# Kernel optimization log

Hardware: AMD Instinct MI355X
Metric: run time of the kernel (lower is better)

The kernel has to match this reference:

```python
import jax, jax.numpy as jnp
import numpy as np

V, N = 3, 32768
C2, C3 = 256, 32          # feat_ch_2D, feat_ch_3D
H = W = 128               # 2D feature map size
D = 32                    # 3D volume feature size
CIN = C2 + C3             # 288, MLP in_channels


def setup_inputs() -> dict:
    key = jax.random.key(0)
    ks = jax.random.split(key, 16)
    sc = 0.02
    inp = {
        'pts': jax.random.uniform(ks[0], (1, N, 3), minval=-0.5, maxval=0.5),
        'pts_proj': jax.random.uniform(ks[1], (1, N, 2), minval=-1.0, maxval=1.0),
        'img_feat0': jax.random.normal(ks[2], (V, C2, H, W)),
        'img_feat1': jax.random.normal(ks[3], (V, C2, H, W)),
        'vol_feat0': jax.random.normal(ks[4], (V, C3, D, D, D)),
        'vol_feat1': jax.random.normal(ks[5], (V, C3, D, D, D)),
        'W0': jax.random.normal(ks[6], (1024, CIN)) * sc,  'b0': jnp.zeros((1024,)),
        'W1': jax.random.normal(ks[7], (512, CIN + 1024)) * sc, 'b1': jnp.zeros((512,)),
        'W2': jax.random.normal(ks[8], (256, CIN + 512)) * sc,  'b2': jnp.zeros((256,)),
        'W3': jax.random.normal(ks[9], (128, CIN + 256)) * sc,  'b3': jnp.zeros((128,)),
        'W4': jax.random.normal(ks[10], (1, 128)) * sc,         'b4': jnp.zeros((1,)),
        'mean_num': 3,
    }
    return inp


def _gs2d(feat, gx, gy):
    # feat: [C,H,W]; gx,gy: [N] normalized coords in [-1,1]
    C, Hh, Ww = feat.shape
    ix = jnp.clip(((gx + 1.0) * Ww - 1.0) * 0.5, 0.0, Ww - 1.0)  # align_corners=False, border pad
    iy = jnp.clip(((gy + 1.0) * Hh - 1.0) * 0.5, 0.0, Hh - 1.0)
    x0f, y0f = jnp.floor(ix), jnp.floor(iy)
    wx, wy = ix - x0f, iy - y0f
    x0 = x0f.astype(jnp.int32); x1 = jnp.minimum(x0 + 1, Ww - 1)
    y0 = y0f.astype(jnp.int32); y1 = jnp.minimum(y0 + 1, Hh - 1)
    v00 = feat[:, y0, x0]; v01 = feat[:, y0, x1]
    v10 = feat[:, y1, x0]; v11 = feat[:, y1, x1]
    return (v00 * (1 - wy) * (1 - wx) + v01 * (1 - wy) * wx
            + v10 * wy * (1 - wx) + v11 * wy * wx)  # [C,N]


def _gs3d(feat, gx, gy, gz):
    # feat: [C,D,H,W]; grid x->W, y->H, z->D (torch grid_sample convention)
    C, Dd, Hh, Ww = feat.shape
    ix = jnp.clip(((gx + 1.0) * Ww - 1.0) * 0.5, 0.0, Ww - 1.0)
    iy = jnp.clip(((gy + 1.0) * Hh - 1.0) * 0.5, 0.0, Hh - 1.0)
    iz = jnp.clip(((gz + 1.0) * Dd - 1.0) * 0.5, 0.0, Dd - 1.0)
    x0f, y0f, z0f = jnp.floor(ix), jnp.floor(iy), jnp.floor(iz)
    wx, wy, wz = ix - x0f, iy - y0f, iz - z0f
    x0 = x0f.astype(jnp.int32); x1 = jnp.minimum(x0 + 1, Ww - 1)
    y0 = y0f.astype(jnp.int32); y1 = jnp.minimum(y0 + 1, Hh - 1)
    z0 = z0f.astype(jnp.int32); z1 = jnp.minimum(z0 + 1, Dd - 1)
    def g(zi, yi, xi):
        return feat[:, zi, yi, xi]  # [C,N]
    out = (g(z0, y0, x0) * (1 - wz) * (1 - wy) * (1 - wx)
           + g(z0, y0, x1) * (1 - wz) * (1 - wy) * wx
           + g(z0, y1, x0) * (1 - wz) * wy * (1 - wx)
           + g(z0, y1, x1) * (1 - wz) * wy * wx
           + g(z1, y0, x0) * wz * (1 - wy) * (1 - wx)
           + g(z1, y0, x1) * wz * (1 - wy) * wx
           + g(z1, y1, x0) * wz * wy * (1 - wx)
           + g(z1, y1, x1) * wz * wy * wx)
    return out  # [C,N]


def _lrelu(x):
    return jnp.where(x >= 0, x, 0.2 * x)


def _conv1x1(Wm, bm, x):
    # x: [V,C,N] -> [V,O,N]
    return jnp.einsum('oc,vcn->von', Wm, x) + bm[None, :, None]


def _mlp0(x, W0, b0, W1, b1, W2, b2, W3, b3):
    out = _lrelu(_conv1x1(W0, b0, x))
    out = _lrelu(_conv1x1(W1, b1, jnp.concatenate([x, out], axis=1)))
    out = _lrelu(_conv1x1(W2, b2, jnp.concatenate([x, out], axis=1)))
    out = _lrelu(_conv1x1(W3, b3, jnp.concatenate([x, out], axis=1)))
    return out  # [V,128,N]


def _forward(pts, pts_proj, img_feats, vol_feats,
             W0, b0, W1, b1, W2, b2, W3, b3, W4, b4, mean_num):
    v = img_feats[0].shape[0]
    gx2 = jnp.broadcast_to(pts_proj[:, :, 0], (v, pts_proj.shape[1]))
    gy2 = jnp.broadcast_to(pts_proj[:, :, 1], (v, pts_proj.shape[1]))
    p = pts * 2.0  # pts *= 2.0 before 3D sampling
    gx3 = jnp.broadcast_to(p[:, :, 0], (v, p.shape[1]))
    gy3 = jnp.broadcast_to(p[:, :, 1], (v, p.shape[1]))
    gz3 = jnp.broadcast_to(p[:, :, 2], (v, p.shape[1]))
    outs = []
    for img_feat, vol_feat in zip(img_feats, vol_feats):
        f2 = jax.vmap(_gs2d)(img_feat, gx2, gy2)            # [V,C2,N]
        f3 = jax.vmap(_gs3d)(vol_feat, gx3, gy3, gz3)       # [V,C3,N]
        pt_feat = jnp.concatenate([f2, f3], axis=1)         # [V,288,N]
        pt_out0 = _mlp0(pt_feat, W0, b0, W1, b1, W2, b2, W3, b3)
        pt_out0_mean = jnp.mean(pt_out0[:mean_num], axis=0, keepdims=True)  # [1,128,N]
        sdf = jax.nn.sigmoid(_conv1x1(W4, b4, pt_out0_mean))                # [1,1,N]
        outs.append(jnp.transpose(sdf, (0, 2, 1)))                          # [1,N,1]
    return tuple(outs)


def reference(pts, pts_proj, img_feat0, img_feat1, vol_feat0, vol_feat1,
              W0, b0, W1, b1, W2, b2, W3, b3, W4, b4, mean_num):
    return _forward(pts, pts_proj, [img_feat0, img_feat1], [vol_feat0, vol_feat1],
                    W0, b0, W1, b1, W2, b2, W3, b3, W4, b4, mean_num)
```

## Files before the change

### kernel.cpp

```cpp
#include <hip/hip_runtime.h>
#include <hip/hip_bf16.h>

#define NV 3
#define NPTS 32768
#define C2C 256
#define C3C 32
#define CINC 288
#define CINP 320
#define HH 128
#define WWW 128
#define DDD 32

typedef short bh8 __attribute__((ext_vector_type(8)));
typedef float fx4 __attribute__((ext_vector_type(4)));
typedef unsigned short us4 __attribute__((ext_vector_type(4)));

__device__ __forceinline__ float b2f(unsigned short u) {
    unsigned int x = ((unsigned int)u) << 16;
    return __uint_as_float(x);
}
__device__ __forceinline__ unsigned short f2b(float f) {
    unsigned int x = __float_as_uint(f);
    unsigned int r = (x + 0x7FFFu + ((x >> 16) & 1u)) >> 16;
    return (unsigned short)r;
}

__device__ __forceinline__ void gl2lds16(const unsigned short* g, unsigned short* l) {
    __builtin_amdgcn_global_load_lds(
        (const __attribute__((address_space(1))) unsigned int*)g,
        (__attribute__((address_space(3))) unsigned int*)l, 16, 0, 0);
}

__device__ __forceinline__ int xcd_swz(int orig, int nwg) {
    int xcd = orig & 7;
    int q = nwg >> 3, r = nwg & 7;
    int base = (xcd < r) ? xcd * (q + 1) : r * (q + 1) + (xcd - r) * q;
    return base + (orig >> 3);
}

__global__ void k_wpad(const float* __restrict__ src, unsigned short* __restrict__ dst, int M, int Kp) {
    int idx = blockIdx.x * 256 + threadIdx.x;
    if (idx >= M * Kp) return;
    int m = idx / Kp, k = idx - m * Kp;
    int Ksrc = Kp - 32;
    float v;
    if (k < CINC) v = src[(size_t)m * Ksrc + k];
    else if (k < CINP) v = 0.0f;
    else v = src[(size_t)m * Ksrc + (k - 32)];
    dst[idx] = f2b(v);
}

__global__ void k_timg(const float* __restrict__ in, unsigned short* __restrict__ out) {
    int v = blockIdx.x >> 7, y = blockIdx.x & 127;
    int x0 = blockIdx.y << 6, c0 = blockIdx.z << 6;
    __shared__ float t[64][65];
    int tx = threadIdx.x & 63, tg = threadIdx.x >> 6;
    const float* src = in + (((size_t)(v * C2C + c0) * HH + y) * WWW + x0);
#pragma unroll
    for (int i = 0; i < 16; i++) {
        int cl = tg * 16 + i;
        t[cl][tx] = src[(size_t)cl * (HH * WWW) + tx];
    }
    __syncthreads();
    unsigned short* dst = out + ((size_t)(v * HH + y) * WWW + x0) * C2C + c0;
#pragma unroll
    for (int i = 0; i < 16; i++) {
        int xl = tg * 16 + i;
        dst[(size_t)xl * C2C + tx] = f2b(t[tx][xl]);
    }
}

__global__ void k_tvol(const float* __restrict__ in, unsigned short* __restrict__ out) {
    int v = blockIdx.x;
    int s0 = blockIdx.y << 8;
    __shared__ float t[32][257];
    int tid = threadIdx.x;
    const float* src = in + (size_t)v * C3C * 32768 + s0;
#pragma unroll
    for (int c = 0; c < 32; c++) t[c][tid] = src[(size_t)c * 32768 + tid];
    __syncthreads();
    unsigned short* dst = out + ((size_t)v * 32768 + s0) * C3C;
    int c = tid & 31, sb = tid >> 5;
#pragma unroll
    for (int j = 0; j < 32; j++) {
        int sl = j * 8 + sb;
        dst[(size_t)sl * C3C + c] = f2b(t[c][sl]);
    }
}

__global__ __launch_bounds__(256) void k_sample(const float* __restrict__ pts, const float* __restrict__ proj,
                         const unsigned short* __restrict__ imgT, const unsigned short* __restrict__ volT,
                         unsigned short* __restrict__ ptT, int n0, int Nk) {
    int w = threadIdx.x >> 6, l = threadIdx.x & 63;
    int i = blockIdx.x * 4 + w;
    int v = blockIdx.y;
    int n = n0 + i;
    unsigned short* dstRow = ptT + (size_t)(v * Nk + i) * CINP;

    {
        float gx = proj[n * 2 + 0], gy = proj[n * 2 + 1];
        float ix = fminf(fmaxf(((gx + 1.0f) * (float)WWW - 1.0f) * 0.5f, 0.0f), (float)(WWW - 1));
        float iy = fminf(fmaxf(((gy + 1.0f) * (float)HH - 1.0f) * 0.5f, 0.0f), (float)(HH - 1));
        float x0f = floorf(ix), y0f = floorf(iy);
        float wx = ix - x0f, wy = iy - y0f;
        int x0 = (int)x0f, y0 = (int)y0f;
        int x1 = min(x0 + 1, WWW - 1), y1 = min(y0 + 1, HH - 1);
        const unsigned short* base = imgT + (size_t)v * HH * WWW * C2C;
        us4 a = *((const us4*)(base + ((size_t)(y0 * WWW + x0)) * C2C) + l);
        us4 b = *((const us4*)(base + ((size_t)(y0 * WWW + x1)) * C2C) + l);
        us4 c = *((const us4*)(base + ((size_t)(y1 * WWW + x0)) * C2C) + l);
        us4 d = *((const us4*)(base + ((size_t)(y1 * WWW + x1)) * C2C) + l);
        float w00 = (1.0f - wy) * (1.0f - wx), w01 = (1.0f - wy) * wx;
        float w10 = wy * (1.0f - wx), w11 = wy * wx;
        us4 rv;
#pragma unroll
        for (int r = 0; r < 4; r++) {
            float f = b2f(a[r]) * w00 + b2f(b[r]) * w01 + b2f(c[r]) * w10 + b2f(d[r]) * w11;
            rv[r] = f2b(f);
        }
        *(us4*)(dstRow + l * 4) = rv;
    }
    {
        float gx = pts[n * 3 + 0] * 2.0f, gy = pts[n * 3 + 1] * 2.0f, gz = pts[n * 3 + 2] * 2.0f;
        float ix = fminf(fmaxf(((gx + 1.0f) * (float)DDD - 1.0f) * 0.5f, 0.0f), (float)(DDD - 1));
        float iy = fminf(fmaxf(((gy + 1.0f) * (float)DDD - 1.0f) * 0.5f, 0.0f), (float)(DDD - 1));
        float iz = fminf(fmaxf(((gz + 1.0f) * (float)DDD - 1.0f) * 0.5f, 0.0f), (float)(DDD - 1));
        float x0f = floorf(ix), y0f = floorf(iy), z0f = floorf(iz);
        float wx = ix - x0f, wy = iy - y0f, wz = iz - z0f;
        int x0 = (int)x0f, y0 = (int)y0f, z0 = (int)z0f;
        int x1 = min(x0 + 1, DDD - 1), y1 = min(y0 + 1, DDD - 1), z1 = min(z0 + 1, DDD - 1);
        int c = l & 31, zs = l >> 5;
        int zi = zs ? z1 : z0;
        float wzs = zs ? wz : (1.0f - wz);
        const unsigned short* base = volT + (size_t)v * 32768 * C3C;
        float f00 = b2f(base[((size_t)((zi * 32 + y0) * 32 + x0)) * C3C + c]);
        float f01 = b2f(base[((size_t)((zi * 32 + y0) * 32 + x1)) * C3C + c]);
        float f10 = b2f(base[((size_t)((zi * 32 + y1) * 32 + x0)) * C3C + c]);
        float f11 = b2f(base[((size_t)((zi * 32 + y1) * 32 + x1)) * C3C + c]);
        float r = (f00 * (1.0f - wy) * (1.0f - wx) + f01 * (1.0f - wy) * wx +
                   f10 * wy * (1.0f - wx) + f11 * wy * wx) * wzs;
        float other = __shfl_xor(r, 32);
        r += other;
        if (zs == 0) dstRow[C2C + c] = f2b(r);
    }
    if (l < 8) *(us4*)(dstRow + CINC + l * 4) = (us4){0, 0, 0, 0};
}

template <int K1, int K2, int M>
__device__ __forceinline__ void gemm128_body(const unsigned short* __restrict__ A,
                                             const unsigned short* __restrict__ B1,
                                             const unsigned short* __restrict__ B2,
                                             const float* __restrict__ bias,
                                             unsigned short* __restrict__ C) {
    constexpr int K = K1 + K2;
    __shared__ unsigned short Ash[128 * 32];
    __shared__ unsigned short Bsh[128 * 32];
    int tid = threadIdx.x;
    int w = tid >> 6, l = tid & 63;
    int la = l & 15, lg = l >> 4;
    int wm = w & 1, wn = w >> 1;
    int gx = gridDim.x;
    int nwg = gx * gridDim.y;
    int bid = xcd_swz(blockIdx.y * gx + blockIdx.x, nwg);
    int mBlk = (bid % gx) * 128;
    int nBlk = (bid / gx) * 128;

    int sRow = l >> 2;
    int sCol = (l & 3) * 8;

    fx4 acc[4][4];
#pragma unroll
    for (int mi = 0; mi < 4; mi++)
#pragma unroll
        for (int ni = 0; ni < 4; ni++) acc[mi][ni] = (fx4){0.f, 0.f, 0.f, 0.f};

    const unsigned short* Ag = A + (size_t)mBlk * K;
    {
        const unsigned short* Bg = B1 + (size_t)nBlk * K1;
        for (int k0 = 0; k0 < K1; k0 += 32) {
#pragma unroll
            for (int j = 0; j < 2; j++) {
                int r = w * 32 + j * 16 + sRow;
                gl2lds16(Ag + (size_t)r * K + k0 + sCol, &Ash[r * 32 + sCol]);
                gl2lds16(Bg + (size_t)r * K1 + k0 + sCol, &Bsh[r * 32 + sCol]);
            }
            __syncthreads();
            bh8 af[4], bfv[4];
#pragma unroll
            for (int mi = 0; mi < 4; mi++) af[mi] = *(const bh8*)&Ash[(wm * 64 + mi * 16 + la) * 32 + lg * 8];
#pragma unroll
            for (int ni = 0; ni < 4; ni++) bfv[ni] = *(const bh8*)&Bsh[(wn * 64 + ni * 16 + la) * 32 + lg * 8];
#pragma unroll
            for (int mi = 0; mi < 4; mi++)
#pragma unroll
                for (int ni = 0; ni < 4; ni++)
                    acc[mi][ni] = __builtin_amdgcn_mfma_f32_16x16x32_bf16(af[mi], bfv[ni], acc[mi][ni], 0, 0, 0);
            __syncthreads();
        }
    }
    if constexpr (K2 > 0) {
        const unsigned short* Bg = B2 + (size_t)nBlk * K2;
        for (int k0 = 0; k0 < K2; k0 += 32) {
#pragma unroll
            for (int j = 0; j < 2; j++) {
                int r = w * 32 + j * 16 + sRow;
                gl2lds16(Ag + (size_t)r * K + K1 + k0 + sCol, &Ash[r * 32 + sCol]);
                gl2lds16(Bg + (size_t)r * K2 + k0 + sCol, &Bsh[r * 32 + sCol]);
            }
            __syncthreads();
            bh8 af[4], bfv[4];
#pragma unroll
            for (int mi = 0; mi < 4; mi++) af[mi] = *(const bh8*)&Ash[(wm * 64 + mi * 16 + la) * 32 + lg * 8];
#pragma unroll
            for (int ni = 0; ni < 4; ni++) bfv[ni] = *(const bh8*)&Bsh[(wn * 64 + ni * 16 + la) * 32 + lg * 8];
#pragma unroll
            for (int mi = 0; mi < 4; mi++)
#pragma unroll
                for (int ni = 0; ni < 4; ni++)
                    acc[mi][ni] = __builtin_amdgcn_mfma_f32_16x16x32_bf16(af[mi], bfv[ni], acc[mi][ni], 0, 0, 0);
            __syncthreads();
        }
    }

#pragma unroll
    for (int mi = 0; mi < 4; mi++) {
        int m0 = mBlk + wm * 64 + mi * 16 + lg * 4;
        fx4 bb = *(const fx4*)(bias + m0);
#pragma unroll
        for (int ni = 0; ni < 4; ni++) {
            int n = nBlk + wn * 64 + ni * 16 + la;
            us4 rv;
#pragma unroll
            for (int r = 0; r < 4; r++) {
                float x = acc[mi][ni][r] + bb[r];
                x = (x >= 0.0f) ? x : 0.2f * x;
                rv[r] = f2b(x);
            }
            *(us4*)(C + (size_t)n * M + m0) = rv;
        }
    }
}

__global__ __launch_bounds__(256) void k_g0(const unsigned short* __restrict__ A, const unsigned short* __restrict__ B1,
                                            const float* __restrict__ bias, unsigned short* __restrict__ C) {
    gemm128_body<320, 0, 1024>(A, B1, nullptr, bias, C);
}
__global__ __launch_bounds__(256) void k_g2(const unsigned short* __restrict__ A, const unsigned short* __restrict__ B1,
                                            const unsigned short* __restrict__ B2, const float* __restrict__ bias,
                                            unsigned short* __restrict__ C) {
    gemm128_body<320, 512, 256>(A, B1, B2, bias, C);
}
__global__ __launch_bounds__(256) void k_g3(const unsigned short* __restrict__ A, const unsigned short* __restrict__ B1,
                                            const unsigned short* __restrict__ B2, const float* __restrict__ bias,
                                            unsigned short* __restrict__ C) {
    gemm128_body<320, 256, 128>(A, B1, B2, bias, C);
}

__global__ __launch_bounds__(512) void k_g1(const unsigned short* __restrict__ A,
                                            const unsigned short* __restrict__ B1,
                                            const unsigned short* __restrict__ B2,
                                            const float* __restrict__ bias,
                                            unsigned short* __restrict__ C, int nOff) {
    constexpr int Kp = 1344;
    constexpr int K2 = 1024;
    constexpr int M = 512;
    constexpr int nt = Kp >> 6;
    __shared__ unsigned short As[2][256 * 64];
    __shared__ unsigned short Bs[2][256 * 64];
    int tid = threadIdx.x;
    int w = tid >> 6, l = tid & 63;
    int la = l & 15, lg = l >> 4;
    int wm = w >> 2, wn = w & 3;
    int gx = gridDim.x;
    int nwg = gx * gridDim.y;
    int bid = xcd_swz(blockIdx.y * gx + blockIdx.x, nwg);
    int mBlk = (bid % gx) * 256;
    int nBlk = (bid / gx) * 256 + nOff;

    const unsigned short* Ag = A + (size_t)mBlk * Kp;

    fx4 acc[8][4];
#pragma unroll
    for (int mi = 0; mi < 8; mi++)
#pragma unroll
        for (int ni = 0; ni < 4; ni++) acc[mi][ni] = (fx4){0.f, 0.f, 0.f, 0.f};

    auto burst = [&](int t, int nxt) {
        const unsigned short* bsrc;
        size_t ldb;
        int kc;
        if (t < 5) { bsrc = B1; ldb = CINP; kc = t * 64; }
        else       { bsrc = B2; ldb = (size_t)K2; kc = (t - 5) * 64; }
        bsrc += (size_t)nBlk * ldb + kc;
        const unsigned short* asrc = Ag + t * 64;
#pragma unroll
        for (int h = 0; h < 2; h++)
#pragma unroll
            for (int j = 0; j < 2; j++) {
                int idx = j * 512 + tid;
                int r = (h << 7) + (idx >> 3);
                int c = (idx & 7) ^ (r & 7);
                gl2lds16(asrc + (size_t)r * Kp + c * 8, &As[nxt][(h << 13) + idx * 8]);
            }
#pragma unroll
        for (int h = 0; h < 2; h++)
#pragma unroll
            for (int j = 0; j < 2; j++) {
                int idx = j * 512 + tid;
                int r = (h << 7) + (idx >> 3);
                int c = (idx & 7) ^ (r & 7);
                gl2lds16(bsrc + (size_t)r * ldb + c * 8, &Bs[nxt][(h << 13) + idx * 8]);
            }
    };

    burst(0, 0);
    asm volatile("s_waitcnt vmcnt(0)" ::: "memory");
    __builtin_amdgcn_s_barrier();
    for (int t = 0; t < nt; t++) {
        int cur = t & 1;
        const unsigned short* Ab = &As[cur][0];
        const unsigned short* Bb = &Bs[cur][0];
        bh8 afr[4][2];
#pragma unroll
        for (int p = 0; p < 4; p++) {
            int qm = p >> 1, qn = p & 1;
            if (qn == 0) {
#pragma unroll
                for (int m2 = 0; m2 < 4; m2++)
#pragma unroll
                    for (int s = 0; s < 2; s++) {
                        int row = wm * 128 + (qm * 4 + m2) * 16 + la;
                        int c = (s * 4 + lg) ^ (row & 7);
                        afr[m2][s] = *(const bh8*)&Ab[row * 64 + c * 8];
                    }
            }
            bh8 bfr[2][2];
#pragma unroll
            for (int n2 = 0; n2 < 2; n2++)
#pragma unroll
                for (int s = 0; s < 2; s++) {
                    int row = wn * 64 + (qn * 2 + n2) * 16 + la;
                    int c = (s * 4 + lg) ^ (row & 7);
                    bfr[n2][s] = *(const bh8*)&Bb[row * 64 + c * 8];
                }
            __builtin_amdgcn_s_barrier();
            __builtin_amdgcn_s_setprio(1);
#pragma unroll
            for (int m2 = 0; m2 < 4; m2++)
#pragma unroll
                for (int n2 = 0; n2 < 2; n2++)
#pragma unroll
                    for (int s = 0; s < 2; s++)
                        acc[qm * 4 + m2][qn * 2 + n2] = __builtin_amdgcn_mfma_f32_16x16x32_bf16(
                            afr[m2][s], bfr[n2][s], acc[qm * 4 + m2][qn * 2 + n2], 0, 0, 0);
            __builtin_amdgcn_s_setprio(0);
            if (p == 0 && t + 1 < nt) burst(t + 1, cur ^ 1);
            if (p == 3) {
                asm volatile("s_waitcnt lgkmcnt(0)" ::: "memory");
                if (t + 1 < nt) asm volatile("s_waitcnt vmcnt(8)" ::: "memory");
            }
            __builtin_amdgcn_s_barrier();
        }
    }

#pragma unroll
    for (int mi = 0; mi < 8; mi++) {
        int m0 = mBlk + wm * 128 + mi * 16 + lg * 4;
        fx4 bb = *(const fx4*)(bias + m0);
#pragma unroll
        for (int ni = 0; ni < 4; ni++) {
            int n = nBlk + wn * 64 + ni * 16 + la;
            us4 rv;
#pragma unroll
            for (int r = 0; r < 4; r++) {
                float x = acc[mi][ni][r] + bb[r];
                x = (x >= 0.0f) ? x : 0.2f * x;
                rv[r] = f2b(x);
            }
            *(us4*)(C + (size_t)n * M + m0) = rv;
        }
    }
}

__global__ __launch_bounds__(256) void k_head(const unsigned short* __restrict__ o3, const float* __restrict__ W4,
                       const float* __restrict__ b4, const int* __restrict__ mn_p,
                       float* __restrict__ out, int n0, int Nk, int level) {
    int wv = threadIdx.x >> 6, l = threadIdx.x & 63;
    int sub = l >> 4, cl = l & 15;
    int i = blockIdx.x * 16 + wv * 4 + sub;
    if (i >= Nk) return;
    int mn = *mn_p;
    if (mn > NV) mn = NV;
    if (mn < 1) mn = 1;
    fx4 w0 = *(const fx4*)(W4 + cl * 8);
    fx4 w1 = *(const fx4*)(W4 + cl * 8 + 4);
    float s = 0.0f;
    for (int v = 0; v < mn; v++) {
        bh8 x = *(const bh8*)(o3 + (size_t)(v * Nk + i) * 128 + cl * 8);
#pragma unroll
        for (int r = 0; r < 4; r++) s += w0[r] * b2f((unsigned short)x[r]);
#pragma unroll
        for (int r = 0; r < 4; r++) s += w1[r] * b2f((unsigned short)x[4 + r]);
    }
#pragma unroll
    for (int m = 1; m < 16; m <<= 1) s += __shfl_xor(s, m);
    if (cl == 0) {
        s = s / (float)mn + b4[0];
        out[(size_t)level * NPTS + n0 + i] = 1.0f / (1.0f + expf(-s));
    }
}

extern "C" void kernel_launch(void* const* d_in, const int* in_sizes, int n_in,
                              void* d_out, int out_size, void* d_ws, size_t ws_size,
                              hipStream_t stream) {
    const float* pts = (const float*)d_in[0];
    const float* proj = (const float*)d_in[1];
    const float* img[2] = {(const float*)d_in[2], (const float*)d_in[3]};
    const float* vol[2] = {(const float*)d_in[4], (const float*)d_in[5]};
    const float* Wf[4] = {(const float*)d_in[6], (const float*)d_in[8], (const float*)d_in[10], (const float*)d_in[12]};
    const float* bf[4] = {(const float*)d_in[7], (const float*)d_in[9], (const float*)d_in[11], (const float*)d_in[13]};
    const float* W4 = (const float*)d_in[14];
    const float* b4 = (const float*)d_in[15];
    const int* mn = (const int*)d_in[16];
    float* out = (float*)d_out;

    const int Kp[4] = {320, 1344, 832, 576};
    const int Msz[4] = {1024, 512, 256, 128};

    char* ws = (char*)d_ws;
    size_t off = 0;
    auto alloc = [&](size_t bytes) -> char* {
        char* p = ws + off;
        off = (off + bytes + 255) & ~(size_t)255;
        return p;
    };

    unsigned short* Wb[4];
    for (int i = 0; i < 4; i++) Wb[i] = (unsigned short*)alloc((size_t)Msz[i] * Kp[i] * 2);
    unsigned short* imgT = (unsigned short*)alloc((size_t)NV * HH * WWW * C2C * 2);
    unsigned short* volT = (unsigned short*)alloc((size_t)NV * 32768 * C3C * 2);
    size_t fixed = off;

    const size_t perPt = (size_t)NV * 2 * (CINP + 1024 + 512 + 256 + 128);
    int Nk = NPTS;
    if (fixed + (size_t)Nk * perPt + 4096 > ws_size) {
        size_t avail = (ws_size > fixed + 4096) ? (ws_size - fixed - 4096) : 0;
        long nk = (long)(avail / perPt);
        nk = (nk / 512) * 512;
        if (nk < 512) nk = 512;
        if (nk > NPTS) nk = NPTS;
        Nk = (int)nk;
    }
    unsigned short* ptT = (unsigned short*)alloc((size_t)NV * Nk * CINP * 2);
    unsigned short* o0 = (unsigned short*)alloc((size_t)NV * Nk * 1024 * 2);
    unsigned short* o1 = (unsigned short*)alloc((size_t)NV * Nk * 512 * 2);
    unsigned short* o2 = (unsigned short*)alloc((size_t)NV * Nk * 256 * 2);
    unsigned short* o3 = (unsigned short*)alloc((size_t)NV * Nk * 128 * 2);

    for (int i = 0; i < 4; i++) {
        int n = Msz[i] * Kp[i];
        k_wpad<<<(n + 255) / 256, 256, 0, stream>>>(Wf[i], Wb[i], Msz[i], Kp[i]);
    }

    for (int lvl = 0; lvl < 2; lvl++) {
        k_timg<<<dim3(NV * HH, WWW / 64, C2C / 64), 256, 0, stream>>>(img[lvl], imgT);
        k_tvol<<<dim3(NV, 32768 / 256), 256, 0, stream>>>(vol[lvl], volT);
        for (int n0 = 0; n0 < NPTS; n0 += Nk) {
            int nk = NPTS - n0 < Nk ? NPTS - n0 : Nk;
            int NC = NV * nk;
            int NH = NC / 2;
            k_sample<<<dim3(nk / 4, NV), 256, 0, stream>>>(pts, proj, imgT, volT, ptT, n0, nk);
            k_g0<<<dim3(1024 / 128, NC / 128), 256, 0, stream>>>(Wb[0], ptT, bf[0], o0);
            k_g1<<<dim3(512 / 256, NH / 256), 512, 0, stream>>>(Wb[1], ptT, o0, bf[1], o1, 0);
            k_g1<<<dim3(512 / 256, NH / 256), 512, 0, stream>>>(Wb[1], ptT, o0, bf[1], o1, NH);
            k_g2<<<dim3(256 / 128, NC / 128), 256, 0, stream>>>(Wb[2], ptT, o1, bf[2], o2);
            k_g3<<<dim3(128 / 128, NC / 128), 256, 0, stream>>>(Wb[3], ptT, o2, bf[3], o3);
            k_head<<<(nk + 15) / 16, 256, 0, stream>>>(o3, W4, b4, mn, out, n0, nk, lvl);
        }
    }
}
```

Before: 1.089 ms.

## Double-buffer GEMM tiles, split k_g1 staging, merge launches and reuse buffers

The small GEMM body now double-buffers its LDS tiles and prefetches the next K tile while running MFMAs on the current one, replacing the sync-per-tile loop. k_g1 spreads its global-to-LDS loads across three phases with finer vmcnt waits and runs as one launch instead of two halves. The weight padding and the image and volume transposes for both levels are each merged into single launches, and the o2/o3 buffers alias o0 to shrink the workspace. This uses more LDS and changes wait-count accounting, which risks races if the counts are wrong.

```diff
diff --git a/kernel.cpp b/kernel.cpp
--- a/kernel.cpp
+++ b/kernel.cpp
@@ -38,9 +38,18 @@
     return base + (orig >> 3);
 }
 
-__global__ void k_wpad(const float* __restrict__ src, unsigned short* __restrict__ dst, int M, int Kp) {
+__global__ void k_wpad4(const float* __restrict__ s0, const float* __restrict__ s1,
+                        const float* __restrict__ s2, const float* __restrict__ s3,
+                        unsigned short* __restrict__ d0, unsigned short* __restrict__ d1,
+                        unsigned short* __restrict__ d2, unsigned short* __restrict__ d3) {
+    const int Ms[4] = {1024, 512, 256, 128};
+    const int Kps[4] = {320, 1344, 832, 576};
+    int i = blockIdx.y;
+    int M = Ms[i], Kp = Kps[i];
     int idx = blockIdx.x * 256 + threadIdx.x;
     if (idx >= M * Kp) return;
+    const float* src = (i == 0) ? s0 : (i == 1) ? s1 : (i == 2) ? s2 : s3;
+    unsigned short* dst = (i == 0) ? d0 : (i == 1) ? d1 : (i == 2) ? d2 : d3;
     int m = idx / Kp, k = idx - m * Kp;
     int Ksrc = Kp - 32;
     float v;
@@ -50,9 +59,12 @@
     dst[idx] = f2b(v);
 }
 
-__global__ void k_timg(const float* __restrict__ in, unsigned short* __restrict__ out) {
+__global__ void k_timg(const float* __restrict__ in0, const float* __restrict__ in1,
+                       unsigned short* __restrict__ out, size_t lvlStride) {
+    int lvl = blockIdx.z >> 2, cb = blockIdx.z & 3;
+    const float* in = lvl ? in1 : in0;
     int v = blockIdx.x >> 7, y = blockIdx.x & 127;
-    int x0 = blockIdx.y << 6, c0 = blockIdx.z << 6;
+    int x0 = blockIdx.y << 6, c0 = cb << 6;
     __shared__ float t[64][65];
     int tx = threadIdx.x & 63, tg = threadIdx.x >> 6;
     const float* src = in + (((size_t)(v * C2C + c0) * HH + y) * WWW + x0);
@@ -62,7 +74,7 @@
         t[cl][tx] = src[(size_t)cl * (HH * WWW) + tx];
     }
     __syncthreads();
-    unsigned short* dst = out + ((size_t)(v * HH + y) * WWW + x0) * C2C + c0;
+    unsigned short* dst = out + lvl * lvlStride + ((size_t)(v * HH + y) * WWW + x0) * C2C + c0;
 #pragma unroll
     for (int i = 0; i < 16; i++) {
         int xl = tg * 16 + i;
@@ -70,7 +82,10 @@
     }
 }
 
-__global__ void k_tvol(const float* __restrict__ in, unsigned short* __restrict__ out) {
+__global__ void k_tvol(const float* __restrict__ in0, const float* __restrict__ in1,
+                       unsigned short* __restrict__ out, size_t lvlStride) {
+    int lvl = blockIdx.z;
+    const float* in = lvl ? in1 : in0;
     int v = blockIdx.x;
     int s0 = blockIdx.y << 8;
     __shared__ float t[32][257];
@@ -79,7 +94,7 @@
 #pragma unroll
     for (int c = 0; c < 32; c++) t[c][tid] = src[(size_t)c * 32768 + tid];
     __syncthreads();
-    unsigned short* dst = out + ((size_t)v * 32768 + s0) * C3C;
+    unsigned short* dst = out + lvl * lvlStride + ((size_t)v * 32768 + s0) * C3C;
     int c = tid & 31, sb = tid >> 5;
 #pragma unroll
     for (int j = 0; j < 32; j++) {
@@ -146,15 +161,18 @@
     if (l < 8) *(us4*)(dstRow + CINC + l * 4) = (us4){0, 0, 0, 0};
 }
 
-template <int K1, int K2, int M>
+template <int K2, int M>
 __device__ __forceinline__ void gemm128_body(const unsigned short* __restrict__ A,
                                              const unsigned short* __restrict__ B1,
                                              const unsigned short* __restrict__ B2,
                                              const float* __restrict__ bias,
                                              unsigned short* __restrict__ C) {
+    constexpr int K1 = CINP;
     constexpr int K = K1 + K2;
-    __shared__ unsigned short Ash[128 * 32];
-    __shared__ unsigned short Bsh[128 * 32];
+    constexpr int nt1 = K1 / 32;
+    constexpr int nt = K / 32;
+    __shared__ unsigned short Ash[2][128 * 32];
+    __shared__ unsigned short Bsh[2][128 * 32];
     int tid = threadIdx.x;
     int w = tid >> 6, l = tid & 63;
     int la = l & 15, lg = l >> 4;
@@ -164,9 +182,12 @@
     int bid = xcd_swz(blockIdx.y * gx + blockIdx.x, nwg);
     int mBlk = (bid % gx) * 128;
     int nBlk = (bid / gx) * 128;
-
-    int sRow = l >> 2;
-    int sCol = (l & 3) * 8;
+    int sRow = l >> 2, sCol = (l & 3) * 8;
+    int r0 = w * 32 + sRow, r1 = r0 + 16;
+
+    const unsigned short* Ag = A + (size_t)mBlk * K;
+    const unsigned short* B1g = B1 + (size_t)nBlk * K1;
+    const unsigned short* B2g = (K2 > 0) ? (B2 + (size_t)nBlk * K2) : (const unsigned short*)0;
 
     fx4 acc[4][4];
 #pragma unroll
@@ -174,52 +195,37 @@
 #pragma unroll
         for (int ni = 0; ni < 4; ni++) acc[mi][ni] = (fx4){0.f, 0.f, 0.f, 0.f};
 
-    const unsigned short* Ag = A + (size_t)mBlk * K;
-    {
-        const unsigned short* Bg = B1 + (size_t)nBlk * K1;
-        for (int k0 = 0; k0 < K1; k0 += 32) {
-#pragma unroll
-            for (int j = 0; j < 2; j++) {
-                int r = w * 32 + j * 16 + sRow;
-                gl2lds16(Ag + (size_t)r * K + k0 + sCol, &Ash[r * 32 + sCol]);
-                gl2lds16(Bg + (size_t)r * K1 + k0 + sCol, &Bsh[r * 32 + sCol]);
-            }
-            __syncthreads();
-            bh8 af[4], bfv[4];
-#pragma unroll
-            for (int mi = 0; mi < 4; mi++) af[mi] = *(const bh8*)&Ash[(wm * 64 + mi * 16 + la) * 32 + lg * 8];
-#pragma unroll
-            for (int ni = 0; ni < 4; ni++) bfv[ni] = *(const bh8*)&Bsh[(wn * 64 + ni * 16 + la) * 32 + lg * 8];
-#pragma unroll
-            for (int mi = 0; mi < 4; mi++)
-#pragma unroll
-                for (int ni = 0; ni < 4; ni++)
-                    acc[mi][ni] = __builtin_amdgcn_mfma_f32_16x16x32_bf16(af[mi], bfv[ni], acc[mi][ni], 0, 0, 0);
-            __syncthreads();
-        }
-    }
-    if constexpr (K2 > 0) {
-        const unsigned short* Bg = B2 + (size_t)nBlk * K2;
-        for (int k0 = 0; k0 < K2; k0 += 32) {
-#pragma unroll
-            for (int j = 0; j < 2; j++) {
-                int r = w * 32 + j * 16 + sRow;
-                gl2lds16(Ag + (size_t)r * K + K1 + k0 + sCol, &Ash[r * 32 + sCol]);
-                gl2lds16(Bg + (size_t)r * K2 + k0 + sCol, &Bsh[r * 32 + sCol]);
-            }
-            __syncthreads();
-            bh8 af[4], bfv[4];
-#pragma unroll
-            for (int mi = 0; mi < 4; mi++) af[mi] = *(const bh8*)&Ash[(wm * 64 + mi * 16 + la) * 32 + lg * 8];
-#pragma unroll
-            for (int ni = 0; ni < 4; ni++) bfv[ni] = *(const bh8*)&Bsh[(wn * 64 + ni * 16 + la) * 32 + lg * 8];
-#pragma unroll
-            for (int mi = 0; mi < 4; mi++)
-#pragma unroll
-                for (int ni = 0; ni < 4; ni++)
-                    acc[mi][ni] = __builtin_amdgcn_mfma_f32_16x16x32_bf16(af[mi], bfv[ni], acc[mi][ni], 0, 0, 0);
-            __syncthreads();
-        }
+    auto stage = [&](int t, int nxt) {
+        const unsigned short* as = Ag + t * 32 + sCol;
+        gl2lds16(as + (size_t)r0 * K, &Ash[nxt][r0 * 32 + sCol]);
+        gl2lds16(as + (size_t)r1 * K, &Ash[nxt][r1 * 32 + sCol]);
+        const unsigned short* bs;
+        size_t ldb;
+        if (t < nt1) { bs = B1g + t * 32 + sCol; ldb = (size_t)K1; }
+        else         { bs = B2g + (t - nt1) * 32 + sCol; ldb = (size_t)K2; }
+        gl2lds16(bs + (size_t)r0 * ldb, &Bsh[nxt][r0 * 32 + sCol]);
+        gl2lds16(bs + (size_t)r1 * ldb, &Bsh[nxt][r1 * 32 + sCol]);
+    };
+
+    stage(0, 0);
+    asm volatile("s_waitcnt vmcnt(0)" ::: "memory");
+    __builtin_amdgcn_s_barrier();
+    for (int t = 0; t < nt; t++) {
+        int cur = t & 1;
+        if (t + 1 < nt) stage(t + 1, cur ^ 1);
+        bh8 af[4], bfv[4];
+#pragma unroll
+        for (int mi = 0; mi < 4; mi++) af[mi] = *(const bh8*)&Ash[cur][(wm * 64 + mi * 16 + la) * 32 + lg * 8];
+#pragma unroll
+        for (int ni = 0; ni < 4; ni++) bfv[ni] = *(const bh8*)&Bsh[cur][(wn * 64 + ni * 16 + la) * 32 + lg * 8];
+#pragma unroll
+        for (int mi = 0; mi < 4; mi++)
+#pragma unroll
+            for (int ni = 0; ni < 4; ni++)
+                acc[mi][ni] = __builtin_amdgcn_mfma_f32_16x16x32_bf16(af[mi], bfv[ni], acc[mi][ni], 0, 0, 0);
+        asm volatile("s_waitcnt lgkmcnt(0)" ::: "memory");
+        if (t + 1 < nt) asm volatile("s_waitcnt vmcnt(0)" ::: "memory");
+        __builtin_amdgcn_s_barrier();
     }
 
 #pragma unroll
@@ -243,24 +249,24 @@
 
 __global__ __launch_bounds__(256) void k_g0(const unsigned short* __restrict__ A, const unsigned short* __restrict__ B1,
                                             const float* __restrict__ bias, unsigned short* __restrict__ C) {
-    gemm128_body<320, 0, 1024>(A, B1, nullptr, bias, C);
+    gemm128_body<0, 1024>(A, B1, nullptr, bias, C);
 }
 __global__ __launch_bounds__(256) void k_g2(const unsigned short* __restrict__ A, const unsigned short* __restrict__ B1,
                                             const unsigned short* __restrict__ B2, const float* __restrict__ bias,
                                             unsigned short* __restrict__ C) {
-    gemm128_body<320, 512, 256>(A, B1, B2, bias, C);
+    gemm128_body<512, 256>(A, B1, B2, bias, C);
 }
 __global__ __launch_bounds__(256) void k_g3(const unsigned short* __restrict__ A, const unsigned short* __restrict__ B1,
                                             const unsigned short* __restrict__ B2, const float* __restrict__ bias,
                                             unsigned short* __restrict__ C) {
-    gemm128_body<320, 256, 128>(A, B1, B2, bias, C);
+    gemm128_body<256, 128>(A, B1, B2, bias, C);
 }
 
 __global__ __launch_bounds__(512) void k_g1(const unsigned short* __restrict__ A,
                                             const unsigned short* __restrict__ B1,
                                             const unsigned short* __restrict__ B2,
                                             const float* __restrict__ bias,
-                                            unsigned short* __restrict__ C, int nOff) {
+                                            unsigned short* __restrict__ C) {
     constexpr int Kp = 1344;
     constexpr int K2 = 1024;
     constexpr int M = 512;
@@ -275,7 +281,7 @@
     int nwg = gx * gridDim.y;
     int bid = xcd_swz(blockIdx.y * gx + blockIdx.x, nwg);
     int mBlk = (bid % gx) * 256;
-    int nBlk = (bid / gx) * 256 + nOff;
+    int nBlk = (bid / gx) * 256;
 
     const unsigned short* Ag = A + (size_t)mBlk * Kp;
 
@@ -285,23 +291,13 @@
 #pragma unroll
         for (int ni = 0; ni < 4; ni++) acc[mi][ni] = (fx4){0.f, 0.f, 0.f, 0.f};
 
-    auto burst = [&](int t, int nxt) {
+    auto stageB = [&](int t, int nxt) {
         const unsigned short* bsrc;
         size_t ldb;
         int kc;
         if (t < 5) { bsrc = B1; ldb = CINP; kc = t * 64; }
         else       { bsrc = B2; ldb = (size_t)K2; kc = (t - 5) * 64; }
         bsrc += (size_t)nBlk * ldb + kc;
-        const unsigned short* asrc = Ag + t * 64;
-#pragma unroll
-        for (int h = 0; h < 2; h++)
-#pragma unroll
-            for (int j = 0; j < 2; j++) {
-                int idx = j * 512 + tid;
-                int r = (h << 7) + (idx >> 3);
-                int c = (idx & 7) ^ (r & 7);
-                gl2lds16(asrc + (size_t)r * Kp + c * 8, &As[nxt][(h << 13) + idx * 8]);
-            }
 #pragma unroll
         for (int h = 0; h < 2; h++)
 #pragma unroll
@@ -312,10 +308,33 @@
                 gl2lds16(bsrc + (size_t)r * ldb + c * 8, &Bs[nxt][(h << 13) + idx * 8]);
             }
     };
-
-    burst(0, 0);
+    auto stageA1 = [&](int t, int nxt) {
+        const unsigned short* asrc = Ag + t * 64;
+#pragma unroll
+        for (int h = 0; h < 2; h++) {
+            int idx = tid;
+            int r = (h << 7) + (idx >> 3);
+            int c = (idx & 7) ^ (r & 7);
+            gl2lds16(asrc + (size_t)r * Kp + c * 8, &As[nxt][(h << 13) + idx * 8]);
+        }
+    };
+    auto stageA2 = [&](int t, int nxt) {
+        const unsigned short* asrc = Ag + t * 64;
+#pragma unroll
+        for (int h = 0; h < 2; h++) {
+            int idx = 512 + tid;
+            int r = (h << 7) + (idx >> 3);
+            int c = (idx & 7) ^ (r & 7);
+            gl2lds16(asrc + (size_t)r * Kp + c * 8, &As[nxt][(h << 13) + idx * 8]);
+        }
+    };
+
+    stageB(0, 0);
+    stageA1(0, 0);
+    stageA2(0, 0);
     asm volatile("s_waitcnt vmcnt(0)" ::: "memory");
     __builtin_amdgcn_s_barrier();
+
     for (int t = 0; t < nt; t++) {
         int cur = t & 1;
         const unsigned short* Ab = &As[cur][0];
@@ -343,6 +362,9 @@
                     int c = (s * 4 + lg) ^ (row & 7);
                     bfr[n2][s] = *(const bh8*)&Bb[row * 64 + c * 8];
                 }
+            if (p == 0 && t + 1 < nt) stageB(t + 1, cur ^ 1);
+            if (p == 1 && t + 1 < nt) stageA1(t + 1, cur ^ 1);
+            if (p == 2 && t + 1 < nt) stageA2(t + 1, cur ^ 1);
             __builtin_amdgcn_s_barrier();
             __builtin_amdgcn_s_setprio(1);
 #pragma unroll
@@ -354,10 +376,13 @@
                         acc[qm * 4 + m2][qn * 2 + n2] = __builtin_amdgcn_mfma_f32_16x16x32_bf16(
                             afr[m2][s], bfr[n2][s], acc[qm * 4 + m2][qn * 2 + n2], 0, 0, 0);
             __builtin_amdgcn_s_setprio(0);
-            if (p == 0 && t + 1 < nt) burst(t + 1, cur ^ 1);
+            if (p == 1) {
+                if (t + 1 < nt) asm volatile("s_waitcnt vmcnt(6)" ::: "memory");
+                else            asm volatile("s_waitcnt vmcnt(0)" ::: "memory");
+            }
             if (p == 3) {
                 asm volatile("s_waitcnt lgkmcnt(0)" ::: "memory");
-                if (t + 1 < nt) asm volatile("s_waitcnt vmcnt(8)" ::: "memory");
+                if (t + 1 < nt) asm volatile("s_waitcnt vmcnt(2)" ::: "memory");
             }
             __builtin_amdgcn_s_barrier();
         }
@@ -435,13 +460,16 @@
         return p;
     };
 
+    const size_t imgStride = (size_t)NV * HH * WWW * C2C;
+    const size_t volStride = (size_t)NV * 32768 * C3C;
+
     unsigned short* Wb[4];
     for (int i = 0; i < 4; i++) Wb[i] = (unsigned short*)alloc((size_t)Msz[i] * Kp[i] * 2);
-    unsigned short* imgT = (unsigned short*)alloc((size_t)NV * HH * WWW * C2C * 2);
-    unsigned short* volT = (unsigned short*)alloc((size_t)NV * 32768 * C3C * 2);
+    unsigned short* imgT = (unsigned short*)alloc(2 * imgStride * 2);
+    unsigned short* volT = (unsigned short*)alloc(2 * volStride * 2);
     size_t fixed = off;
 
-    const size_t perPt = (size_t)NV * 2 * (CINP + 1024 + 512 + 256 + 128);
+    const size_t perPt = (size_t)NV * 2 * (CINP + 1024 + 512);
     int Nk = NPTS;
     if (fixed + (size_t)Nk * perPt + 4096 > ws_size) {
         size_t avail = (ws_size > fixed + 4096) ? (ws_size - fixed - 4096) : 0;
@@ -454,25 +482,21 @@
     unsigned short* ptT = (unsigned short*)alloc((size_t)NV * Nk * CINP * 2);
     unsigned short* o0 = (unsigned short*)alloc((size_t)NV * Nk * 1024 * 2);
     unsigned short* o1 = (unsigned short*)alloc((size_t)NV * Nk * 512 * 2);
-    unsigned short* o2 = (unsigned short*)alloc((size_t)NV * Nk * 256 * 2);
-    unsigned short* o3 = (unsigned short*)alloc((size_t)NV * Nk * 128 * 2);
-
-    for (int i = 0; i < 4; i++) {
-        int n = Msz[i] * Kp[i];
-        k_wpad<<<(n + 255) / 256, 256, 0, stream>>>(Wf[i], Wb[i], Msz[i], Kp[i]);
-    }
+    unsigned short* o2 = o0;
+    unsigned short* o3 = o0 + (size_t)NV * Nk * 256;
+
+    k_wpad4<<<dim3(2688, 4), 256, 0, stream>>>(Wf[0], Wf[1], Wf[2], Wf[3], Wb[0], Wb[1], Wb[2], Wb[3]);
+    k_timg<<<dim3(NV * HH, WWW / 64, 8), 256, 0, stream>>>(img[0], img[1], imgT, imgStride);
+    k_tvol<<<dim3(NV, 32768 / 256, 2), 256, 0, stream>>>(vol[0], vol[1], volT, volStride);
 
     for (int lvl = 0; lvl < 2; lvl++) {
-        k_timg<<<dim3(NV * HH, WWW / 64, C2C / 64), 256, 0, stream>>>(img[lvl], imgT);
-        k_tvol<<<dim3(NV, 32768 / 256), 256, 0, stream>>>(vol[lvl], volT);
         for (int n0 = 0; n0 < NPTS; n0 += Nk) {
             int nk = NPTS - n0 < Nk ? NPTS - n0 : Nk;
             int NC = NV * nk;
-            int NH = NC / 2;
-            k_sample<<<dim3(nk / 4, NV), 256, 0, stream>>>(pts, proj, imgT, volT, ptT, n0, nk);
+            k_sample<<<dim3(nk / 4, NV), 256, 0, stream>>>(pts, proj, imgT + lvl * imgStride,
+                                                           volT + lvl * volStride, ptT, n0, nk);
             k_g0<<<dim3(1024 / 128, NC / 128), 256, 0, stream>>>(Wb[0], ptT, bf[0], o0);
-            k_g1<<<dim3(512 / 256, NH / 256), 512, 0, stream>>>(Wb[1], ptT, o0, bf[1], o1, 0);
-            k_g1<<<dim3(512 / 256, NH / 256), 512, 0, stream>>>(Wb[1], ptT, o0, bf[1], o1, NH);
+            k_g1<<<dim3(512 / 256, NC / 256), 512, 0, stream>>>(Wb[1], ptT, o0, bf[1], o1);
             k_g2<<<dim3(256 / 128, NC / 128), 256, 0, stream>>>(Wb[2], ptT, o1, bf[2], o2);
             k_g3<<<dim3(128 / 128, NC / 128), 256, 0, stream>>>(Wb[3], ptT, o2, bf[3], o3);
             k_head<<<(nk + 15) / 16, 256, 0, stream>>>(o3, W4, b4, mn, out, n0, nk, lvl);
```

Result: faster. 1.065 ms (-2.2%).
